# Optimization experiments

Hardware: AMD Instinct MI355X
Metric: run time of the kernel (lower is better)

Reference implementation:

```python
import jax, jax.numpy as jnp
import numpy as np

NG, ND, CIN = 100000, 50000, 128
H, D = 8, 32
HID = H * D
E = 200000
SCALE = 1.0 / np.sqrt(D)


def _segment_softmax(logits, seg, num):
    # logits: [E, H]; softmax over edges sharing the same destination node
    m = jax.ops.segment_max(logits, seg, num_segments=num)
    m = jnp.where(jnp.isfinite(m), m, 0.0)  # guard empty segments
    e = jnp.exp(logits - m[seg])
    s = jax.ops.segment_sum(e, seg, num_segments=num)
    return e / (s[seg] + 1e-16)


def _kqv(x, Wk, bk, Wq, bq, Wv, bv):
    n = x.shape[0]
    return ((x @ Wk + bk).reshape(n, H, D),
            (x @ Wq + bq).reshape(n, H, D),
            (x @ Wv + bv).reshape(n, H, D))


def _message(k_src, v_src, q_dst, src, dst, a_rel, m_rel, p_rel, n_dst):
    # per-edge-type relation transform of gathered K/V, softmax over dst, scatter-add
    k_e = jnp.einsum('ehd,hdf->ehf', k_src[src], a_rel)          # [E,H,D]
    v_e = jnp.einsum('ehd,hdf->ehf', v_src[src], m_rel)          # [E,H,D]
    logits = jnp.einsum('ehf,ehf->eh', q_dst[dst], k_e) * p_rel * SCALE
    alpha = _segment_softmax(logits, dst, n_dst)                 # [E,H]
    return jax.ops.segment_sum(alpha[..., None] * v_e, dst, num_segments=n_dst)


def _forward(x_gene, x_disease, Win_g, bin_g, Wk_g, bk_g, Wq_g, bq_g, Wv_g, bv_g,
             Wa_g, ba_g, skip_g, Win_d, bin_d, Wk_d, bk_d, Wq_d, bq_d, Wv_d, bv_d,
             Wa_d, ba_d, skip_d, a_g2d, m_g2d, p_g2d, a_d2g, m_d2g, p_d2g,
             a_g2g, m_g2g, p_g2g, prelu_w,
             g2d_src, g2d_dst, d2g_src, d2g_dst, g2g_src, g2g_dst):
    # per-type input projection (Encoder.lin_dict)
    xg = x_gene @ Win_g + bin_g      # [NG, HID]
    xd = x_disease @ Win_d + bin_d   # [ND, HID]
    ng, nd = xg.shape[0], xd.shape[0]
    kg, qg, vg = _kqv(xg, Wk_g, bk_g, Wq_g, bq_g, Wv_g, bv_g)
    kd, qd, vd = _kqv(xd, Wk_d, bk_d, Wq_d, bq_d, Wv_d, bv_d)
    # HGTConv: message passing per edge type, summed per destination type
    out_d = _message(kg, vg, qd, g2d_src, g2d_dst, a_g2d, m_g2d, p_g2d, nd)
    out_g = (_message(kd, vd, qg, d2g_src, d2g_dst, a_d2g, m_d2g, p_d2g, ng)
             + _message(kg, vg, qg, g2g_src, g2g_dst, a_g2g, m_g2g, p_g2g, ng))

    def finish(out, x_proj, Wa, ba, skip):
        h = jax.nn.gelu(out.reshape(-1, HID), approximate=False) @ Wa + ba
        beta = jax.nn.sigmoid(skip)
        h = beta * h + (1.0 - beta) * x_proj          # HGT skip connection
        return jnp.where(h > 0, h, prelu_w * h)       # PReLU; Dropout=identity (eval)

    return (finish(out_g, xg, Wa_g, ba_g, skip_g),
            finish(out_d, xd, Wa_d, ba_d, skip_d))


def setup_inputs():
    key = jax.random.key(0)
    ki = iter(jax.random.split(key, 64))
    def nrm(shape, s):
        return (jax.random.normal(next(ki), shape) * s).astype(jnp.float32)
    inp = {}
    inp['x_gene'] = jax.random.normal(next(ki), (NG, CIN), jnp.float32)
    inp['x_disease'] = jax.random.normal(next(ki), (ND, CIN), jnp.float32)
    for t in ('g', 'd'):
        inp[f'Win_{t}'] = nrm((CIN, HID), 0.09)
        inp[f'bin_{t}'] = jnp.zeros((HID,), jnp.float32)
        for p in ('k', 'q', 'v'):
            inp[f'W{p}_{t}'] = nrm((HID, HID), 0.06)
            inp[f'b{p}_{t}'] = jnp.zeros((HID,), jnp.float32)
        inp[f'Wa_{t}'] = nrm((HID, HID), 0.06)
        inp[f'ba_{t}'] = jnp.zeros((HID,), jnp.float32)
        inp[f'skip_{t}'] = jnp.ones((1,), jnp.float32)
    for r in ('g2d', 'd2g', 'g2g'):
        inp[f'a_{r}'] = nrm((H, D, D), 0.18)
        inp[f'm_{r}'] = nrm((H, D, D), 0.18)
        inp[f'p_{r}'] = jnp.ones((H,), jnp.float32)
    inp['prelu_w'] = jnp.full((HID,), 0.25, jnp.float32)
    sizes = {'g2d': (NG, ND), 'd2g': (ND, NG), 'g2g': (NG, NG)}
    for r, (ns_, nd_) in sizes.items():
        inp[f'{r}_src'] = jax.random.randint(next(ki), (E,), 0, ns_, jnp.int32)
        inp[f'{r}_dst'] = jax.random.randint(next(ki), (E,), 0, nd_, jnp.int32)
    return inp


def reference(x_gene, x_disease, Win_g, bin_g, Wk_g, bk_g, Wq_g, bq_g, Wv_g, bv_g,
              Wa_g, ba_g, skip_g, Win_d, bin_d, Wk_d, bk_d, Wq_d, bq_d, Wv_d, bv_d,
              Wa_d, ba_d, skip_d, a_g2d, m_g2d, p_g2d, a_d2g, m_d2g, p_d2g,
              a_g2g, m_g2g, p_g2g, prelu_w,
              g2d_src, g2d_dst, d2g_src, d2g_dst, g2g_src, g2g_dst):
    return _forward(x_gene, x_disease, Win_g, bin_g, Wk_g, bk_g, Wq_g, bq_g, Wv_g, bv_g,
                    Wa_g, ba_g, skip_g, Win_d, bin_d, Wk_d, bk_d, Wq_d, bq_d, Wv_d, bv_d,
                    Wa_d, ba_d, skip_d, a_g2d, m_g2d, p_g2d, a_d2g, m_d2g, p_d2g,
                    a_g2g, m_g2g, p_g2g, prelu_w,
                    g2d_src, g2d_dst, d2g_src, d2g_dst, g2g_src, g2g_dst)
```

## Files before the change

### kernel.cpp

```cpp
#include <hip/hip_runtime.h>
#include <hip/hip_bf16.h>
#include <math.h>

typedef unsigned short u16;
typedef __attribute__((ext_vector_type(4))) float f32x4;
typedef __attribute__((ext_vector_type(8))) short s16x8;

__device__ __forceinline__ float b2f(u16 u){
  union { unsigned u; float f; } v; v.u = ((unsigned)u) << 16; return v.f;
}
__device__ __forceinline__ u16 f2b(float f){
  union { float f; unsigned u; } v; v.f = f;
  unsigned r = v.u + 0x7fffu + ((v.u >> 16) & 1u);
  return (u16)(r >> 16);
}

__device__ __forceinline__ void gload_lds(const u16* g, u16* l){
  __builtin_amdgcn_global_load_lds(
      (const __attribute__((address_space(1))) unsigned*)g,
      (__attribute__((address_space(3))) unsigned*)l, 16, 0, 0);
}

__device__ __forceinline__ int chunk_swz(int bid, int nwg){
  int q = nwg >> 3, r = nwg & 7;
  int xcd = bid & 7, off = bid >> 3;
  return (xcd < r ? xcd*(q+1) : r*(q+1) + (xcd-r)*q) + off;
}

__global__ void zero_k(int* __restrict__ p, int n){
  int i = blockIdx.x*256 + threadIdx.x;
  if(i < n) p[i] = 0;
}

struct T6 { const float* W[6]; u16* O[6]; int K[6]; };
__global__ void transpose6(T6 a){
  int r = blockIdx.y;
  int idx = blockIdx.x*256 + threadIdx.x;
  int K = a.K[r];
  if(idx < K*256){ int k = idx >> 8, n = idx & 255; a.O[r][n*K + k] = f2b(a.W[r][idx]); }
}

struct F6 { const float* Wk[6]; const float* A[6]; u16* O[6]; };
__global__ void foldw6(F6 fa){
  int r = blockIdx.y;
  int idx = blockIdx.x*256 + threadIdx.x;
  int n = idx >> 8, k = idx & 255;
  int h = n >> 5, f = n & 31;
  const float* Wk = fa.Wk[r]; const float* A = fa.A[r];
  float s = 0.f;
  #pragma unroll 8
  for(int d = 0; d < 32; d++)
    s += Wk[k*256 + h*32 + d] * A[h*1024 + d*32 + f];
  fa.O[r][n*256 + k] = f2b(s);
}

struct Fb6 { const float* bk[6]; const float* A[6]; float* O[6]; };
__global__ void foldb6(Fb6 fa){
  int r = blockIdx.x;
  int n = threadIdx.x;
  int h = n >> 5, f = n & 31;
  float s = 0.f;
  for(int d = 0; d < 32; d++)
    s += fa.bk[r][h*32 + d] * fa.A[r][h*1024 + d*32 + f];
  fa.O[r][n] = s;
}

struct CSR3 {
  const int* src[3]; const int* dst[3]; int n[3];
  int* cnt[3]; int* rs[3]; int* cur[3]; int* col[3]; int* tot[3];
};
__global__ void count3(CSR3 c, int E){
  int r = blockIdx.y;
  int e = blockIdx.x*256 + threadIdx.x;
  if(e < E) atomicAdd(&c.cnt[r][c.dst[r][e]], 1);
}
__global__ void alloc3(CSR3 c){
  int r = blockIdx.y;
  int i = blockIdx.x*256 + threadIdx.x;
  if(i < c.n[r]) c.rs[r][i] = atomicAdd(c.tot[r], c.cnt[r][i]);
}
__global__ void fill3(CSR3 c, int E){
  int r = blockIdx.y;
  int e = blockIdx.x*256 + threadIdx.x;
  if(e < E){
    int d = c.dst[r][e];
    int p = c.rs[r][d] + atomicAdd(&c.cur[r][d], 1);
    c.col[r][p] = c.src[r][e];
  }
}

struct GMD {
  const void* A; const u16* BT; const float* bias; void* C;
  int M, K, lda, ldc, lgy, base, epi;
};
struct GM4 { GMD g[4]; int n, nblk; };

template<int AF>
__global__ __launch_bounds__(256) void gemm_multi(GM4 P){
  __shared__ u16 sh[128*64];
  u16* As = sh;
  u16* Bs = sh + 128*32;
  const int t = threadIdx.x;
  const int l = chunk_swz(blockIdx.x, P.nblk);
  int g = 0;
  #pragma unroll
  for(int i = 1; i < 4; i++) if(i < P.n && l >= P.g[i].base) g = i;
  const GMD d = P.g[g];
  const int local = l - d.base;
  const int x = local >> d.lgy;
  const int y = local & ((1 << d.lgy) - 1);
  const int m0 = x << 7, n0 = y << 7;
  const int M = d.M, K = d.K, lda = d.lda, ldc = d.ldc;
  const int w = t >> 6, lane = t & 63;
  const int wm = (w >> 1) << 6;
  const int wn = (w & 1) << 6;
  const int lr = lane & 15, lq = lane >> 4;
  const int jr = lane >> 2;
  const int sp = lane & 3;
  f32x4 acc[4][4];
  #pragma unroll
  for(int i=0;i<4;i++)
    #pragma unroll
    for(int j=0;j<4;j++) acc[i][j] = (f32x4){0.f,0.f,0.f,0.f};

  for(int k0 = 0; k0 < K; k0 += 32){
    if(AF){
      const float* Af = (const float*)d.A;
      #pragma unroll
      for(int j = 0; j < 2; j++){
        int s = t + j*256;
        int rr = s >> 2, p2 = s & 3;
        int sl = p2 ^ (rr & 3);
        int gm = m0 + rr; if(gm > M-1) gm = M-1;
        const float* gp = Af + (size_t)gm*lda + k0 + sl*8;
        float4 f0 = *(const float4*)gp;
        float4 f1 = *(const float4*)(gp + 4);
        s16x8 v;
        v[0]=(short)f2b(f0.x); v[1]=(short)f2b(f0.y); v[2]=(short)f2b(f0.z); v[3]=(short)f2b(f0.w);
        v[4]=(short)f2b(f1.x); v[5]=(short)f2b(f1.y); v[6]=(short)f2b(f1.z); v[7]=(short)f2b(f1.w);
        *(s16x8*)&As[rr*32 + p2*8] = v;
      }
    } else {
      const u16* Ab = (const u16*)d.A;
      #pragma unroll
      for(int i = 0; i < 2; i++){
        int rr = w*32 + i*16 + jr;
        int sl = sp ^ (rr & 3);
        int gm = m0 + rr; if(gm > M-1) gm = M-1;
        gload_lds(Ab + (size_t)gm*lda + k0 + sl*8, &As[(w*32 + i*16)*32]);
      }
    }
    #pragma unroll
    for(int i = 0; i < 2; i++){
      int rr = w*32 + i*16 + jr;
      int sl = sp ^ (rr & 3);
      gload_lds(d.BT + (size_t)(n0 + rr)*K + k0 + sl*8, &Bs[(w*32 + i*16)*32]);
    }
    __syncthreads();
    s16x8 a[4], b[4];
    #pragma unroll
    for(int mt=0; mt<4; mt++)
      a[mt] = *(const s16x8*)&As[(wm + mt*16 + lr)*32 + ((lq ^ (lr&3)) << 3)];
    #pragma unroll
    for(int nt=0; nt<4; nt++)
      b[nt] = *(const s16x8*)&Bs[(wn + nt*16 + lr)*32 + ((lq ^ (lr&3)) << 3)];
    #pragma unroll
    for(int mt=0; mt<4; mt++)
      #pragma unroll
      for(int nt=0; nt<4; nt++)
        acc[mt][nt] = __builtin_amdgcn_mfma_f32_16x16x32_bf16(a[mt], b[nt], acc[mt][nt], 0, 0, 0);
    __syncthreads();
  }

  if(d.epi == 1){
    float* C = (float*)d.C;
    #pragma unroll
    for(int nt=0; nt<4; nt++){
      const int col = n0 + wn + nt*16 + lr;
      const float bc = d.bias[col];
      #pragma unroll
      for(int mt=0; mt<4; mt++)
        #pragma unroll
        for(int i=0;i<4;i++){
          int row = m0 + wm + mt*16 + lq*4 + i;
          if(row < M) C[(size_t)row*ldc + col] = acc[mt][nt][i] + bc;
        }
    }
  } else {
    u16* C = (u16*)d.C;
    #pragma unroll
    for(int p = 0; p < 2; p++){
      if((w & 1) == p){
        #pragma unroll
        for(int nt=0; nt<4; nt++){
          const int cp = nt*16 + lr;
          const float bc = d.bias[n0 + p*64 + cp];
          #pragma unroll
          for(int mt=0; mt<4; mt++)
            #pragma unroll
            for(int i=0;i<4;i++){
              int row = wm + mt*16 + lq*4 + i;
              int so = (cp >> 3) ^ (row & 7);
              sh[row*64 + so*8 + (cp & 7)] = f2b(acc[mt][nt][i] + bc);
            }
        }
      }
      __syncthreads();
      {
        int row = t >> 1, hh = t & 1;
        if(m0 + row < M){
          u16* dst = C + (size_t)(m0 + row)*ldc + n0 + p*64 + hh*32;
          #pragma unroll
          for(int j=0;j<4;j++){
            int so = (hh*4 + j) ^ (row & 7);
            *(s16x8*)(dst + j*8) = *(const s16x8*)&sh[row*64 + so*8];
          }
        }
      }
      __syncthreads();
    }
  }
}

struct GE { const u16* A; const u16* BT; const float* bias; float* C;
            const u16* X; const float* skip; const float* prelu; int M, base; };
struct GE2 { GE g[2]; int nblk; };

__global__ __launch_bounds__(256) void gemm_epi2(GE2 P){
  __shared__ u16 As[64*32];
  __shared__ u16 Bs[256*32];
  const int t = threadIdx.x;
  const int l = chunk_swz(blockIdx.x, P.nblk);
  const int g = (l >= P.g[1].base) ? 1 : 0;
  const GE d = P.g[g];
  const int m0 = (l - d.base) << 6;
  const int M = d.M;
  const int w = t >> 6, lane = t & 63;
  const int wn = w << 6;
  const int lr = lane & 15, lq = lane >> 4;
  const int jr = lane >> 2, sp = lane & 3;
  f32x4 acc[4][4];
  #pragma unroll
  for(int i=0;i<4;i++)
    #pragma unroll
    for(int j=0;j<4;j++) acc[i][j] = (f32x4){0.f,0.f,0.f,0.f};

  for(int k0 = 0; k0 < 256; k0 += 32){
    {
      int rr = w*16 + jr;
      int sl = sp ^ (rr & 3);
      int gm = m0 + rr; if(gm > M-1) gm = M-1;
      gload_lds(d.A + (size_t)gm*512 + k0 + sl*8, &As[(w*16)*32]);
    }
    #pragma unroll
    for(int i = 0; i < 4; i++){
      int rr = w*64 + i*16 + jr;
      int sl = sp ^ (rr & 3);
      gload_lds(d.BT + (size_t)rr*256 + k0 + sl*8, &Bs[(w*64 + i*16)*32]);
    }
    __syncthreads();
    s16x8 a[4], b[4];
    #pragma unroll
    for(int mt=0; mt<4; mt++)
      a[mt] = *(const s16x8*)&As[(mt*16 + lr)*32 + ((lq ^ (lr&3)) << 3)];
    #pragma unroll
    for(int nt=0; nt<4; nt++)
      b[nt] = *(const s16x8*)&Bs[(wn + nt*16 + lr)*32 + ((lq ^ (lr&3)) << 3)];
    #pragma unroll
    for(int mt=0; mt<4; mt++)
      #pragma unroll
      for(int nt=0; nt<4; nt++)
        acc[mt][nt] = __builtin_amdgcn_mfma_f32_16x16x32_bf16(a[mt], b[nt], acc[mt][nt], 0, 0, 0);
    __syncthreads();
  }

  const float beta = 1.f/(1.f + __expf(-d.skip[0]));
  #pragma unroll
  for(int nt=0; nt<4; nt++){
    const int col = wn + nt*16 + lr;
    const float bc = d.bias[col];
    const float pw = d.prelu[col];
    #pragma unroll
    for(int mt=0; mt<4; mt++){
      #pragma unroll
      for(int i=0;i<4;i++){
        int row = m0 + mt*16 + lq*4 + i;
        if(row < M){
          float v = acc[mt][nt][i] + bc;
          float xv = b2f(d.X[(size_t)row*256 + col]);
          v = beta*v + (1.f - beta)*xv;
          v = v > 0.f ? v : pw*v;
          d.C[(size_t)row*256 + col] = v;
        }
      }
    }
  }
}

template<int NREL>
__global__ __launch_bounds__(256) void message_gelu_k(
    const u16* __restrict__ KV1, const float* __restrict__ p1,
    const int* __restrict__ rs1, const int* __restrict__ cnt1, const int* __restrict__ col1,
    const u16* __restrict__ KV2, const float* __restrict__ p2,
    const int* __restrict__ rs2, const int* __restrict__ cnt2, const int* __restrict__ col2,
    float* __restrict__ Qio, int n_dst)
{
  int node = (blockIdx.x << 2) + (threadIdx.x >> 6);
  if(node >= n_dst) return;
  int lane = threadIdx.x & 63;
  float4 qv = *(const float4*)(Qio + (size_t)node*256 + (lane << 2));
  float q0=qv.x, q1=qv.y, q2=qv.z, q3=qv.w;
  float o0=0.f, o1=0.f, o2=0.f, o3=0.f;
  #pragma unroll
  for(int rel = 0; rel < NREL; rel++){
    const u16* KV = rel ? KV2 : KV1;
    const float* pr = rel ? p2 : p1;
    const int* rs = rel ? rs2 : rs1;
    const int* cn = rel ? cnt2 : cnt1;
    const int* cl = rel ? col2 : col1;
    float ps = pr[lane >> 3] * 0.17677669529663687f;
    float a0=0.f,a1=0.f,a2=0.f,a3=0.f,ss=0.f,mx=-1e30f;
    int r0 = rs[node], deg = cn[node];
    int i = 0;
    for(; i + 2 <= deg; i += 2){
      const u16* e0 = KV + (size_t)cl[r0+i]  *512 + (lane<<2);
      const u16* e1 = KV + (size_t)cl[r0+i+1]*512 + (lane<<2);
      ushort4 ka = *(const ushort4*)e0;
      ushort4 va = *(const ushort4*)(e0 + 256);
      ushort4 kb = *(const ushort4*)e1;
      ushort4 vb = *(const ushort4*)(e1 + 256);
      float da = q0*b2f(ka.x) + q1*b2f(ka.y) + q2*b2f(ka.z) + q3*b2f(ka.w);
      float db = q0*b2f(kb.x) + q1*b2f(kb.y) + q2*b2f(kb.z) + q3*b2f(kb.w);
      da += __shfl_xor(da, 1); da += __shfl_xor(da, 2); da += __shfl_xor(da, 4);
      db += __shfl_xor(db, 1); db += __shfl_xor(db, 2); db += __shfl_xor(db, 4);
      float la = da * ps, lb = db * ps;
      float nm = fmaxf(mx, fmaxf(la, lb));
      float c  = __expf(mx - nm);
      float wa = __expf(la - nm);
      float wb = __expf(lb - nm);
      mx = nm;
      ss = ss*c + wa + wb;
      a0 = a0*c + wa*b2f(va.x) + wb*b2f(vb.x);
      a1 = a1*c + wa*b2f(va.y) + wb*b2f(vb.y);
      a2 = a2*c + wa*b2f(va.z) + wb*b2f(vb.z);
      a3 = a3*c + wa*b2f(va.w) + wb*b2f(vb.w);
    }
    if(i < deg){
      const u16* e0 = KV + (size_t)cl[r0+i]*512 + (lane<<2);
      ushort4 ka = *(const ushort4*)e0;
      ushort4 va = *(const ushort4*)(e0 + 256);
      float da = q0*b2f(ka.x) + q1*b2f(ka.y) + q2*b2f(ka.z) + q3*b2f(ka.w);
      da += __shfl_xor(da, 1); da += __shfl_xor(da, 2); da += __shfl_xor(da, 4);
      float la = da * ps;
      float nm = fmaxf(mx, la);
      float c  = __expf(mx - nm);
      float wa = __expf(la - nm);
      mx = nm;
      ss = ss*c + wa;
      a0 = a0*c + wa*b2f(va.x);
      a1 = a1*c + wa*b2f(va.y);
      a2 = a2*c + wa*b2f(va.z);
      a3 = a3*c + wa*b2f(va.w);
    }
    float inv = 1.f/(ss + 1e-16f);
    o0 += a0*inv; o1 += a1*inv; o2 += a2*inv; o3 += a3*inv;
  }
  const float c = 0.70710678118654752f;
  float g0 = 0.5f*o0*(1.f + erff(o0*c));
  float g1 = 0.5f*o1*(1.f + erff(o1*c));
  float g2 = 0.5f*o2*(1.f + erff(o2*c));
  float g3 = 0.5f*o3*(1.f + erff(o3*c));
  ushort4 ov;
  ov.x = f2b(g0); ov.y = f2b(g1); ov.z = f2b(g2); ov.w = f2b(g3);
  *(ushort4*)((u16*)Qio + (size_t)node*512 + (lane << 2)) = ov;
}

extern "C" void kernel_launch(void* const* d_in, const int* in_sizes, int n_in,
                              void* d_out, int out_size, void* d_ws, size_t ws_size,
                              hipStream_t stream)
{
  (void)n_in; (void)out_size; (void)ws_size;
  #define IN_F32(i) ((const float*)d_in[i])
  #define IN_I32(i) ((const int*)d_in[i])
  const int NG = in_sizes[0] / 128;
  const int ND = in_sizes[1] / 128;
  const int E  = in_sizes[34];

  char* p = (char*)d_ws;
  auto carve = [&](size_t bytes) -> void* {
    void* q = (void*)p; p += (bytes + 255) & ~(size_t)255; return q;
  };
  u16* XG   = (u16*)carve((size_t)NG*256*2);
  u16* XD   = (u16*)carve((size_t)ND*256*2);
  u16* KVG  = (u16*)carve((size_t)NG*512*2);
  u16* KVD  = (u16*)carve((size_t)ND*512*2);
  u16* WTinG = (u16*)carve(256*128*2);
  u16* WTinD = (u16*)carve(256*128*2);
  u16* WTqG  = (u16*)carve(256*256*2);
  u16* WTqD  = (u16*)carve(256*256*2);
  u16* WTaG  = (u16*)carve(256*256*2);
  u16* WTaD  = (u16*)carve(256*256*2);
  u16* KVW[3]; for(int i=0;i<3;i++) KVW[i] = (u16*)carve(512*256*2);
  float* FBV[3]; for(int i=0;i<3;i++) FBV[i] = (float*)carve(512*4);
  const int zn = 2*(ND + 2*NG) + 8;
  int* zone = (int*)carve((size_t)zn*4);
  int* cnt0 = zone;
  int* cnt1 = cnt0 + ND;
  int* cnt2 = cnt1 + NG;
  int* cur0 = cnt2 + NG;
  int* cur1 = cur0 + ND;
  int* cur2 = cur1 + NG;
  int* tot  = cur2 + NG;
  int* rs0 = (int*)carve((size_t)ND*4);
  int* rs1 = (int*)carve((size_t)NG*4);
  int* rs2 = (int*)carve((size_t)NG*4);
  int* col0 = (int*)carve((size_t)E*4);
  int* col1 = (int*)carve((size_t)E*4);
  int* col2 = (int*)carve((size_t)E*4);

  float* QGio = (float*)d_out;
  float* QDio = (float*)d_out + (size_t)NG*256;

  {
    T6 a;
    const int wi[6] = {2,13,6,17,10,21};
    u16* wo[6] = {WTinG, WTinD, WTqG, WTqD, WTaG, WTaD};
    const int kk[6] = {128,128,256,256,256,256};
    for(int i=0;i<6;i++){ a.W[i]=IN_F32(wi[i]); a.O[i]=wo[i]; a.K[i]=kk[i]; }
    transpose6<<<dim3(256,6), 256, 0, stream>>>(a);
  }
  {
    F6 a; Fb6 b;
    const int wk[6] = {4,8,15,19,4,8};
    const int bk[6] = {5,9,16,20,5,9};
    const int am[6] = {24,25,27,28,30,31};
    for(int i=0;i<6;i++){
      a.Wk[i]=IN_F32(wk[i]); a.A[i]=IN_F32(am[i]);
      a.O[i] = KVW[i>>1] + (size_t)(i & 1)*256*256;
      b.bk[i]=IN_F32(bk[i]); b.A[i]=IN_F32(am[i]);
      b.O[i] = FBV[i>>1] + (i & 1)*256;
    }
    foldw6<<<dim3(256,6), 256, 0, stream>>>(a);
    foldb6<<<6, 256, 0, stream>>>(b);
  }
  CSR3 c;
  c.src[0]=IN_I32(34); c.dst[0]=IN_I32(35); c.n[0]=ND;
  c.src[1]=IN_I32(36); c.dst[1]=IN_I32(37); c.n[1]=NG;
  c.src[2]=IN_I32(38); c.dst[2]=IN_I32(39); c.n[2]=NG;
  c.cnt[0]=cnt0; c.cnt[1]=cnt1; c.cnt[2]=cnt2;
  c.cur[0]=cur0; c.cur[1]=cur1; c.cur[2]=cur2;
  c.rs[0]=rs0; c.rs[1]=rs1; c.rs[2]=rs2;
  c.col[0]=col0; c.col[1]=col1; c.col[2]=col2;
  c.tot[0]=tot; c.tot[1]=tot+1; c.tot[2]=tot+2;
  const int eb = (E + 255) / 256;
  const int nb = (NG + 255) / 256;
  zero_k<<<(zn + 255) / 256, 256, 0, stream>>>(zone, zn);
  count3<<<dim3(eb,3), 256, 0, stream>>>(c, E);
  alloc3<<<dim3(nb,3), 256, 0, stream>>>(c);
  fill3<<<dim3(eb,3), 256, 0, stream>>>(c, E);

  const int xg = (NG + 127)/128, xd = (ND + 127)/128;

  {
    GM4 pj{};
    pj.g[0].A = d_in[0]; pj.g[0].BT = WTinG; pj.g[0].bias = IN_F32(3);  pj.g[0].C = XG;
    pj.g[0].M = NG; pj.g[0].K = 128; pj.g[0].lda = 128; pj.g[0].ldc = 256;
    pj.g[0].lgy = 1; pj.g[0].base = 0; pj.g[0].epi = 0;
    pj.g[1].A = d_in[1]; pj.g[1].BT = WTinD; pj.g[1].bias = IN_F32(14); pj.g[1].C = XD;
    pj.g[1].M = ND; pj.g[1].K = 128; pj.g[1].lda = 128; pj.g[1].ldc = 256;
    pj.g[1].lgy = 1; pj.g[1].base = xg*2; pj.g[1].epi = 0;
    pj.n = 2; pj.nblk = xg*2 + xd*2;
    gemm_multi<1><<<pj.nblk, 256, 0, stream>>>(pj);
  }

  {
    GM4 md{};
    md.g[0].A = XD; md.g[0].BT = WTqD;   md.g[0].bias = IN_F32(18); md.g[0].C = QDio;
    md.g[0].M = ND; md.g[0].K = 256; md.g[0].lda = 256; md.g[0].ldc = 256;
    md.g[0].lgy = 1; md.g[0].base = 0; md.g[0].epi = 1;
    int b1 = xd*2;
    md.g[1].A = XG; md.g[1].BT = KVW[0]; md.g[1].bias = FBV[0]; md.g[1].C = KVG;
    md.g[1].M = NG; md.g[1].K = 256; md.g[1].lda = 256; md.g[1].ldc = 512;
    md.g[1].lgy = 2; md.g[1].base = b1; md.g[1].epi = 0;
    int b2 = b1 + xg*4;
    md.g[2].A = XG; md.g[2].BT = WTqG;   md.g[2].bias = IN_F32(7); md.g[2].C = QGio;
    md.g[2].M = NG; md.g[2].K = 256; md.g[2].lda = 256; md.g[2].ldc = 256;
    md.g[2].lgy = 1; md.g[2].base = b2; md.g[2].epi = 1;
    int b3 = b2 + xg*2;
    md.g[3].A = XD; md.g[3].BT = KVW[1]; md.g[3].bias = FBV[1]; md.g[3].C = KVD;
    md.g[3].M = ND; md.g[3].K = 256; md.g[3].lda = 256; md.g[3].ldc = 512;
    md.g[3].lgy = 2; md.g[3].base = b3; md.g[3].epi = 0;
    md.n = 4; md.nblk = b3 + xd*4;
    gemm_multi<0><<<md.nblk, 256, 0, stream>>>(md);
  }

  message_gelu_k<1><<<(ND + 3) / 4, 256, 0, stream>>>(
      KVG, IN_F32(26), rs0, cnt0, col0,
      nullptr, nullptr, nullptr, nullptr, nullptr,
      QDio, ND);

  {
    GM4 k2{};
    k2.g[0].A = XG; k2.g[0].BT = KVW[2]; k2.g[0].bias = FBV[2]; k2.g[0].C = KVG;
    k2.g[0].M = NG; k2.g[0].K = 256; k2.g[0].lda = 256; k2.g[0].ldc = 512;
    k2.g[0].lgy = 2; k2.g[0].base = 0; k2.g[0].epi = 0;
    k2.n = 1; k2.nblk = xg*4;
    gemm_multi<0><<<k2.nblk, 256, 0, stream>>>(k2);
  }

  message_gelu_k<2><<<(NG + 3) / 4, 256, 0, stream>>>(
      KVD, IN_F32(29), rs1, cnt1, col1,
      KVG, IN_F32(32), rs2, cnt2, col2,
      QGio, NG);

  {
    GE2 ep{};
    ep.g[0].A = (const u16*)QGio; ep.g[0].BT = WTaG; ep.g[0].bias = IN_F32(11);
    ep.g[0].C = QGio; ep.g[0].X = XG; ep.g[0].skip = IN_F32(12); ep.g[0].prelu = IN_F32(33);
    ep.g[0].M = NG; ep.g[0].base = 0;
    ep.g[1].A = (const u16*)QDio; ep.g[1].BT = WTaD; ep.g[1].bias = IN_F32(22);
    ep.g[1].C = QDio; ep.g[1].X = XD; ep.g[1].skip = IN_F32(23); ep.g[1].prelu = IN_F32(33);
    ep.g[1].M = ND; ep.g[1].base = (NG + 63)/64;
    ep.nblk = (NG + 63)/64 + (ND + 63)/64;
    gemm_epi2<<<ep.nblk, 256, 0, stream>>>(ep);
  }
  #undef IN_F32
  #undef IN_I32
}
```

Measured before the change: 1.043 ms.

## Double-buffer LDS tiles in bf16 GEMM kernels to overlap loads with MFMA

Adds a two-stage LDS ping-pong to the bf16-input path of gemm_multi and to gemm_epi2. The next K-slice is issued with global_load_lds while MFMAs run on the current slice, using explicit waitcnt, barrier and setprio. This targets global-load latency exposed between iterations, at the cost of doubled shared memory per block, which may reduce occupancy. The fp32-input path is left single-buffered.

```diff
diff --git a/kernel.cpp b/kernel.cpp
--- a/kernel.cpp
+++ b/kernel.cpp
@@ -97,9 +97,7 @@
 
 template<int AF>
 __global__ __launch_bounds__(256) void gemm_multi(GM4 P){
-  __shared__ u16 sh[128*64];
-  u16* As = sh;
-  u16* Bs = sh + 128*32;
+  __shared__ u16 sh[2][128*64];
   const int t = threadIdx.x;
   const int l = chunk_swz(blockIdx.x, P.nblk);
   int g = 0;
@@ -123,8 +121,10 @@
     #pragma unroll
     for(int j=0;j<4;j++) acc[i][j] = (f32x4){0.f,0.f,0.f,0.f};
 
-  for(int k0 = 0; k0 < K; k0 += 32){
-    if(AF){
+  if(AF){
+    u16* As = sh[0];
+    u16* Bs = sh[0] + 128*32;
+    for(int k0 = 0; k0 < K; k0 += 32){
       const float* Af = (const float*)d.A;
       #pragma unroll
       for(int j = 0; j < 2; j++){
@@ -140,36 +140,77 @@
         v[4]=(short)f2b(f1.x); v[5]=(short)f2b(f1.y); v[6]=(short)f2b(f1.z); v[7]=(short)f2b(f1.w);
         *(s16x8*)&As[rr*32 + p2*8] = v;
       }
-    } else {
-      const u16* Ab = (const u16*)d.A;
+      #pragma unroll
+      for(int i = 0; i < 2; i++){
+        int rr = w*32 + i*16 + jr;
+        int sl = sp ^ (rr & 3);
+        gload_lds(d.BT + (size_t)(n0 + rr)*K + k0 + sl*8, &Bs[(w*32 + i*16)*32]);
+      }
+      __syncthreads();
+      s16x8 a[4], b[4];
+      #pragma unroll
+      for(int mt=0; mt<4; mt++)
+        a[mt] = *(const s16x8*)&As[(wm + mt*16 + lr)*32 + ((lq ^ (lr&3)) << 3)];
+      #pragma unroll
+      for(int nt=0; nt<4; nt++)
+        b[nt] = *(const s16x8*)&Bs[(wn + nt*16 + lr)*32 + ((lq ^ (lr&3)) << 3)];
+      #pragma unroll
+      for(int mt=0; mt<4; mt++)
+        #pragma unroll
+        for(int nt=0; nt<4; nt++)
+          acc[mt][nt] = __builtin_amdgcn_mfma_f32_16x16x32_bf16(a[mt], b[nt], acc[mt][nt], 0, 0, 0);
+      __syncthreads();
+    }
+  } else {
+    const u16* Ab = (const u16*)d.A;
+    auto stage = [&](int kk, int bi){
+      u16* As = sh[bi];
+      u16* Bs = sh[bi] + 128*32;
       #pragma unroll
       for(int i = 0; i < 2; i++){
         int rr = w*32 + i*16 + jr;
         int sl = sp ^ (rr & 3);
         int gm = m0 + rr; if(gm > M-1) gm = M-1;
-        gload_lds(Ab + (size_t)gm*lda + k0 + sl*8, &As[(w*32 + i*16)*32]);
-      }
-    }
-    #pragma unroll
-    for(int i = 0; i < 2; i++){
-      int rr = w*32 + i*16 + jr;
-      int sl = sp ^ (rr & 3);
-      gload_lds(d.BT + (size_t)(n0 + rr)*K + k0 + sl*8, &Bs[(w*32 + i*16)*32]);
-    }
-    __syncthreads();
-    s16x8 a[4], b[4];
-    #pragma unroll
-    for(int mt=0; mt<4; mt++)
-      a[mt] = *(const s16x8*)&As[(wm + mt*16 + lr)*32 + ((lq ^ (lr&3)) << 3)];
-    #pragma unroll
-    for(int nt=0; nt<4; nt++)
-      b[nt] = *(const s16x8*)&Bs[(wn + nt*16 + lr)*32 + ((lq ^ (lr&3)) << 3)];
-    #pragma unroll
-    for(int mt=0; mt<4; mt++)
-      #pragma unroll
-      for(int nt=0; nt<4; nt++)
-        acc[mt][nt] = __builtin_amdgcn_mfma_f32_16x16x32_bf16(a[mt], b[nt], acc[mt][nt], 0, 0, 0);
-    __syncthreads();
+        gload_lds(Ab + (size_t)gm*lda + kk + sl*8, &As[(w*32 + i*16)*32]);
+      }
+      #pragma unroll
+      for(int i = 0; i < 2; i++){
+        int rr = w*32 + i*16 + jr;
+        int sl = sp ^ (rr & 3);
+        gload_lds(d.BT + (size_t)(n0 + rr)*K + kk + sl*8, &Bs[(w*32 + i*16)*32]);
+      }
+    };
+    const int nt = K >> 5;
+    int cur = 0;
+    stage(0, 0);
+    asm volatile("s_waitcnt vmcnt(0)" ::: "memory");
+    __builtin_amdgcn_s_barrier();
+    __builtin_amdgcn_sched_barrier(0);
+    for(int ts = 0; ts < nt; ++ts){
+      if(ts + 1 < nt) stage((ts+1) << 5, cur ^ 1);
+      const u16* As = sh[cur];
+      const u16* Bs = sh[cur] + 128*32;
+      s16x8 a[4], b[4];
+      #pragma unroll
+      for(int mt=0; mt<4; mt++)
+        a[mt] = *(const s16x8*)&As[(wm + mt*16 + lr)*32 + ((lq ^ (lr&3)) << 3)];
+      #pragma unroll
+      for(int nn=0; nn<4; nn++)
+        b[nn] = *(const s16x8*)&Bs[(wn + nn*16 + lr)*32 + ((lq ^ (lr&3)) << 3)];
+      asm volatile("s_waitcnt lgkmcnt(0)" ::: "memory");
+      __builtin_amdgcn_sched_barrier(0);
+      __builtin_amdgcn_s_setprio(1);
+      #pragma unroll
+      for(int mt=0; mt<4; mt++)
+        #pragma unroll
+        for(int nn=0; nn<4; nn++)
+          acc[mt][nn] = __builtin_amdgcn_mfma_f32_16x16x32_bf16(a[mt], b[nn], acc[mt][nn], 0, 0, 0);
+      __builtin_amdgcn_s_setprio(0);
+      asm volatile("s_waitcnt vmcnt(0)" ::: "memory");
+      __builtin_amdgcn_s_barrier();
+      __builtin_amdgcn_sched_barrier(0);
+      cur ^= 1;
+    }
   }
 
   if(d.epi == 1){
@@ -187,6 +228,7 @@
         }
     }
   } else {
+    u16* shm = sh[0];
     u16* C = (u16*)d.C;
     #pragma unroll
     for(int p = 0; p < 2; p++){
@@ -201,7 +243,7 @@
             for(int i=0;i<4;i++){
               int row = wm + mt*16 + lq*4 + i;
               int so = (cp >> 3) ^ (row & 7);
-              sh[row*64 + so*8 + (cp & 7)] = f2b(acc[mt][nt][i] + bc);
+              shm[row*64 + so*8 + (cp & 7)] = f2b(acc[mt][nt][i] + bc);
             }
         }
       }
@@ -213,7 +255,7 @@
           #pragma unroll
           for(int j=0;j<4;j++){
             int so = (hh*4 + j) ^ (row & 7);
-            *(s16x8*)(dst + j*8) = *(const s16x8*)&sh[row*64 + so*8];
+            *(s16x8*)(dst + j*8) = *(const s16x8*)&shm[row*64 + so*8];
           }
         }
       }
@@ -227,8 +269,8 @@
 struct GE2 { GE g[2]; int nblk; };
 
 __global__ __launch_bounds__(256) void gemm_epi2(GE2 P){
-  __shared__ u16 As[64*32];
-  __shared__ u16 Bs[256*32];
+  __shared__ u16 Abuf[2][64*32];
+  __shared__ u16 Bbuf[2][256*32];
   const int t = threadIdx.x;
   const int l = chunk_swz(blockIdx.x, P.nblk);
   const int g = (l >= P.g[1].base) ? 1 : 0;
@@ -245,33 +287,49 @@
     #pragma unroll
     for(int j=0;j<4;j++) acc[i][j] = (f32x4){0.f,0.f,0.f,0.f};
 
-  for(int k0 = 0; k0 < 256; k0 += 32){
+  auto stage = [&](int kk, int bi){
     {
       int rr = w*16 + jr;
       int sl = sp ^ (rr & 3);
       int gm = m0 + rr; if(gm > M-1) gm = M-1;
-      gload_lds(d.A + (size_t)gm*512 + k0 + sl*8, &As[(w*16)*32]);
+      gload_lds(d.A + (size_t)gm*512 + kk + sl*8, &Abuf[bi][(w*16)*32]);
     }
     #pragma unroll
     for(int i = 0; i < 4; i++){
       int rr = w*64 + i*16 + jr;
       int sl = sp ^ (rr & 3);
-      gload_lds(d.BT + (size_t)rr*256 + k0 + sl*8, &Bs[(w*64 + i*16)*32]);
-    }
-    __syncthreads();
+      gload_lds(d.BT + (size_t)rr*256 + kk + sl*8, &Bbuf[bi][(w*64 + i*16)*32]);
+    }
+  };
+  int cur = 0;
+  stage(0, 0);
+  asm volatile("s_waitcnt vmcnt(0)" ::: "memory");
+  __builtin_amdgcn_s_barrier();
+  __builtin_amdgcn_sched_barrier(0);
+  for(int ts = 0; ts < 8; ++ts){
+    if(ts + 1 < 8) stage((ts+1) << 5, cur ^ 1);
+    const u16* As = Abuf[cur];
+    const u16* Bs = Bbuf[cur];
     s16x8 a[4], b[4];
     #pragma unroll
     for(int mt=0; mt<4; mt++)
       a[mt] = *(const s16x8*)&As[(mt*16 + lr)*32 + ((lq ^ (lr&3)) << 3)];
     #pragma unroll
-    for(int nt=0; nt<4; nt++)
-      b[nt] = *(const s16x8*)&Bs[(wn + nt*16 + lr)*32 + ((lq ^ (lr&3)) << 3)];
+    for(int nn=0; nn<4; nn++)
+      b[nn] = *(const s16x8*)&Bs[(wn + nn*16 + lr)*32 + ((lq ^ (lr&3)) << 3)];
+    asm volatile("s_waitcnt lgkmcnt(0)" ::: "memory");
+    __builtin_amdgcn_sched_barrier(0);
+    __builtin_amdgcn_s_setprio(1);
     #pragma unroll
     for(int mt=0; mt<4; mt++)
       #pragma unroll
-      for(int nt=0; nt<4; nt++)
-        acc[mt][nt] = __builtin_amdgcn_mfma_f32_16x16x32_bf16(a[mt], b[nt], acc[mt][nt], 0, 0, 0);
-    __syncthreads();
+      for(int nn=0; nn<4; nn++)
+        acc[mt][nn] = __builtin_amdgcn_mfma_f32_16x16x32_bf16(a[mt], b[nn], acc[mt][nn], 0, 0, 0);
+    __builtin_amdgcn_s_setprio(0);
+    asm volatile("s_waitcnt vmcnt(0)" ::: "memory");
+    __builtin_amdgcn_s_barrier();
+    __builtin_amdgcn_sched_barrier(0);
+    cur ^= 1;
   }
 
   const float beta = 1.f/(1.f + __expf(-d.skip[0]));
```

New measurement: 1.018 ms. 1.02x faster.

## Keep A row-tile resident in LDS and sweep all weight panels per block

Applied to the files above, without the earlier changes.

Replaces the multi-GEMM K/Q/V projection launch with a kernel in which each block loads its full 128x256 row strip of the activations into LDS once, then loops over all output column panels, reading B fragments directly from global memory. When workspace allows, the g2g K/V projection goes into a separate buffer and is folded into the same launch, removing a later launch and a second read of XG. The output GEMM likewise keeps its whole A strip in LDS and drops the per-K-step barriers. In exchange it uses much more LDS per block, which lowers occupancy, and it relies on B being served well from cache without staging.

```diff
diff --git a/kernel.cpp b/kernel.cpp
--- a/kernel.cpp
+++ b/kernel.cpp
@@ -93,18 +93,16 @@
   const void* A; const u16* BT; const float* bias; void* C;
   int M, K, lda, ldc, lgy, base, epi;
 };
-struct GM4 { GMD g[4]; int n, nblk; };
+struct GM5 { GMD g[5]; int n, nblk; };
 
 template<int AF>
-__global__ __launch_bounds__(256) void gemm_multi(GM4 P){
-  __shared__ u16 sh[128*64];
-  u16* As = sh;
-  u16* Bs = sh + 128*32;
+__global__ __launch_bounds__(256) void gemm_multi(GM5 P){
+  __shared__ u16 sh[2][128*64];
   const int t = threadIdx.x;
   const int l = chunk_swz(blockIdx.x, P.nblk);
   int g = 0;
   #pragma unroll
-  for(int i = 1; i < 4; i++) if(i < P.n && l >= P.g[i].base) g = i;
+  for(int i = 1; i < 5; i++) if(i < P.n && l >= P.g[i].base) g = i;
   const GMD d = P.g[g];
   const int local = l - d.base;
   const int x = local >> d.lgy;
@@ -115,16 +113,17 @@
   const int wm = (w >> 1) << 6;
   const int wn = (w & 1) << 6;
   const int lr = lane & 15, lq = lane >> 4;
-  const int jr = lane >> 2;
-  const int sp = lane & 3;
   f32x4 acc[4][4];
   #pragma unroll
   for(int i=0;i<4;i++)
     #pragma unroll
     for(int j=0;j<4;j++) acc[i][j] = (f32x4){0.f,0.f,0.f,0.f};
 
-  for(int k0 = 0; k0 < K; k0 += 32){
-    if(AF){
+  {
+    u16* As = sh[0];
+    u16* Bs = sh[0] + 128*32;
+    const int jr = lane >> 2, sp = lane & 3;
+    for(int k0 = 0; k0 < K; k0 += 32){
       const float* Af = (const float*)d.A;
       #pragma unroll
       for(int j = 0; j < 2; j++){
@@ -140,84 +139,173 @@
         v[4]=(short)f2b(f1.x); v[5]=(short)f2b(f1.y); v[6]=(short)f2b(f1.z); v[7]=(short)f2b(f1.w);
         *(s16x8*)&As[rr*32 + p2*8] = v;
       }
-    } else {
-      const u16* Ab = (const u16*)d.A;
       #pragma unroll
       for(int i = 0; i < 2; i++){
         int rr = w*32 + i*16 + jr;
         int sl = sp ^ (rr & 3);
-        int gm = m0 + rr; if(gm > M-1) gm = M-1;
-        gload_lds(Ab + (size_t)gm*lda + k0 + sl*8, &As[(w*32 + i*16)*32]);
-      }
-    }
-    #pragma unroll
-    for(int i = 0; i < 2; i++){
-      int rr = w*32 + i*16 + jr;
-      int sl = sp ^ (rr & 3);
-      gload_lds(d.BT + (size_t)(n0 + rr)*K + k0 + sl*8, &Bs[(w*32 + i*16)*32]);
-    }
-    __syncthreads();
-    s16x8 a[4], b[4];
-    #pragma unroll
-    for(int mt=0; mt<4; mt++)
-      a[mt] = *(const s16x8*)&As[(wm + mt*16 + lr)*32 + ((lq ^ (lr&3)) << 3)];
-    #pragma unroll
-    for(int nt=0; nt<4; nt++)
-      b[nt] = *(const s16x8*)&Bs[(wn + nt*16 + lr)*32 + ((lq ^ (lr&3)) << 3)];
-    #pragma unroll
-    for(int mt=0; mt<4; mt++)
+        gload_lds(d.BT + (size_t)(n0 + rr)*K + k0 + sl*8, &Bs[(w*32 + i*16)*32]);
+      }
+      __syncthreads();
+      s16x8 a[4], b[4];
+      #pragma unroll
+      for(int mt=0; mt<4; mt++)
+        a[mt] = *(const s16x8*)&As[(wm + mt*16 + lr)*32 + ((lq ^ (lr&3)) << 3)];
       #pragma unroll
       for(int nt=0; nt<4; nt++)
-        acc[mt][nt] = __builtin_amdgcn_mfma_f32_16x16x32_bf16(a[mt], b[nt], acc[mt][nt], 0, 0, 0);
-    __syncthreads();
-  }
-
-  if(d.epi == 1){
-    float* C = (float*)d.C;
-    #pragma unroll
-    for(int nt=0; nt<4; nt++){
-      const int col = n0 + wn + nt*16 + lr;
-      const float bc = d.bias[col];
+        b[nt] = *(const s16x8*)&Bs[(wn + nt*16 + lr)*32 + ((lq ^ (lr&3)) << 3)];
       #pragma unroll
       for(int mt=0; mt<4; mt++)
         #pragma unroll
-        for(int i=0;i<4;i++){
-          int row = m0 + wm + mt*16 + lq*4 + i;
-          if(row < M) C[(size_t)row*ldc + col] = acc[mt][nt][i] + bc;
+        for(int nt=0; nt<4; nt++)
+          acc[mt][nt] = __builtin_amdgcn_mfma_f32_16x16x32_bf16(a[mt], b[nt], acc[mt][nt], 0, 0, 0);
+      __syncthreads();
+    }
+  }
+
+  u16* shm = sh[0];
+  u16* C = (u16*)d.C;
+  #pragma unroll
+  for(int p = 0; p < 2; p++){
+    if((w & 1) == p){
+      #pragma unroll
+      for(int nt=0; nt<4; nt++){
+        const int cp = nt*16 + lr;
+        const float bc = d.bias[n0 + p*64 + cp];
+        #pragma unroll
+        for(int mt=0; mt<4; mt++)
+          #pragma unroll
+          for(int i=0;i<4;i++){
+            int row = wm + mt*16 + lq*4 + i;
+            int so = (cp >> 3) ^ (row & 7);
+            shm[row*64 + so*8 + (cp & 7)] = f2b(acc[mt][nt][i] + bc);
+          }
+      }
+    }
+    __syncthreads();
+    {
+      int row = t >> 1, hh = t & 1;
+      if(m0 + row < M){
+        u16* dst = C + (size_t)(m0 + row)*ldc + n0 + p*64 + hh*32;
+        #pragma unroll
+        for(int j=0;j<4;j++){
+          int so = (hh*4 + j) ^ (row & 7);
+          *(s16x8*)(dst + j*8) = *(const s16x8*)&shm[row*64 + so*8];
         }
-    }
-  } else {
-    u16* C = (u16*)d.C;
+      }
+    }
+    __syncthreads();
+  }
+}
+
+struct Panel { const u16* BT; const float* bias; void* C; int ldc, epi; };
+struct Mega { const u16* A[2]; int M[2]; int np[2]; int pb[2]; int split; Panel p[16]; };
+
+__global__ __launch_bounds__(256) void gemm_mega(Mega P){
+  __shared__ u16 As[128*256];
+  __shared__ u16 Cs[128*64];
+  const int t = threadIdx.x;
+  const int blk = blockIdx.x;
+  const int side = (blk >= P.split) ? 1 : 0;
+  const u16* A = P.A[side];
+  const int M = P.M[side];
+  const int np = P.np[side];
+  const int pb = P.pb[side];
+  const int m0 = (side ? blk - P.split : blk) << 7;
+  const int w = t >> 6, lane = t & 63;
+  const int wm = (w >> 1) << 6;
+  const int wn = (w & 1) << 6;
+  const int lr = lane & 15, lq = lane >> 4;
+
+  #pragma unroll
+  for(int i = 0; i < 16; i++){
+    int rbase = w*32 + i*2;
+    int rr = rbase + (lane >> 5);
+    int sp = lane & 31;
+    int sl = sp ^ (rr & 7);
+    int gm = m0 + rr; if(gm > M-1) gm = M-1;
+    gload_lds(A + (size_t)gm*256 + sl*8, &As[rbase*256]);
+  }
+  asm volatile("s_waitcnt vmcnt(0)" ::: "memory");
+  __syncthreads();
+
+  for(int p = 0; p < np; p++){
+    const u16* Bp = P.p[pb + p].BT;
+    const float* bias = P.p[pb + p].bias;
+    void* Cp = P.p[pb + p].C;
+    const int ldc = P.p[pb + p].ldc;
+    const int epi = P.p[pb + p].epi;
+    f32x4 acc[4][4];
     #pragma unroll
-    for(int p = 0; p < 2; p++){
-      if((w & 1) == p){
+    for(int i=0;i<4;i++)
+      #pragma unroll
+      for(int j=0;j<4;j++) acc[i][j] = (f32x4){0.f,0.f,0.f,0.f};
+
+    #pragma unroll 2
+    for(int ts = 0; ts < 8; ts++){
+      s16x8 b[4], a[4];
+      #pragma unroll
+      for(int nt=0;nt<4;nt++)
+        b[nt] = *(const s16x8*)&Bp[(size_t)(wn + nt*16 + lr)*256 + ts*32 + lq*8];
+      #pragma unroll
+      for(int mt=0;mt<4;mt++){
+        int ra = wm + mt*16 + lr;
+        int ps = (ts*4 + lq) ^ (ra & 7);
+        a[mt] = *(const s16x8*)&As[ra*256 + ps*8];
+      }
+      #pragma unroll
+      for(int mt=0;mt<4;mt++)
         #pragma unroll
-        for(int nt=0; nt<4; nt++){
-          const int cp = nt*16 + lr;
-          const float bc = d.bias[n0 + p*64 + cp];
+        for(int nt=0;nt<4;nt++)
+          acc[mt][nt] = __builtin_amdgcn_mfma_f32_16x16x32_bf16(a[mt], b[nt], acc[mt][nt], 0, 0, 0);
+    }
+
+    if(epi == 1){
+      float* C = (float*)Cp;
+      #pragma unroll
+      for(int nt=0; nt<4; nt++){
+        const int col = wn + nt*16 + lr;
+        const float bc = bias[col];
+        #pragma unroll
+        for(int mt=0; mt<4; mt++)
           #pragma unroll
-          for(int mt=0; mt<4; mt++)
+          for(int i=0;i<4;i++){
+            int row = m0 + wm + mt*16 + lq*4 + i;
+            if(row < M) C[(size_t)row*ldc + col] = acc[mt][nt][i] + bc;
+          }
+      }
+    } else {
+      u16* C = (u16*)Cp;
+      #pragma unroll
+      for(int p2 = 0; p2 < 2; p2++){
+        if((w & 1) == p2){
+          #pragma unroll
+          for(int nt=0; nt<4; nt++){
+            const int cp = nt*16 + lr;
+            const float bc = bias[p2*64 + cp];
             #pragma unroll
-            for(int i=0;i<4;i++){
-              int row = wm + mt*16 + lq*4 + i;
-              int so = (cp >> 3) ^ (row & 7);
-              sh[row*64 + so*8 + (cp & 7)] = f2b(acc[mt][nt][i] + bc);
-            }
-        }
-      }
-      __syncthreads();
-      {
-        int row = t >> 1, hh = t & 1;
-        if(m0 + row < M){
-          u16* dst = C + (size_t)(m0 + row)*ldc + n0 + p*64 + hh*32;
-          #pragma unroll
-          for(int j=0;j<4;j++){
-            int so = (hh*4 + j) ^ (row & 7);
-            *(s16x8*)(dst + j*8) = *(const s16x8*)&sh[row*64 + so*8];
+            for(int mt=0; mt<4; mt++)
+              #pragma unroll
+              for(int i=0;i<4;i++){
+                int row = wm + mt*16 + lq*4 + i;
+                int so = (cp >> 3) ^ (row & 7);
+                Cs[row*64 + so*8 + (cp & 7)] = f2b(acc[mt][nt][i] + bc);
+              }
           }
         }
-      }
-      __syncthreads();
+        __syncthreads();
+        {
+          int row = t >> 1, hh = t & 1;
+          if(m0 + row < M){
+            u16* dst = C + (size_t)(m0 + row)*ldc + p2*64 + hh*32;
+            #pragma unroll
+            for(int j=0;j<4;j++){
+              int so = (hh*4 + j) ^ (row & 7);
+              *(s16x8*)(dst + j*8) = *(const s16x8*)&Cs[row*64 + so*8];
+            }
+          }
+        }
+        __syncthreads();
+      }
     }
   }
 }
@@ -227,8 +315,7 @@
 struct GE2 { GE g[2]; int nblk; };
 
 __global__ __launch_bounds__(256) void gemm_epi2(GE2 P){
-  __shared__ u16 As[64*32];
-  __shared__ u16 Bs[256*32];
+  __shared__ u16 As[64*256];
   const int t = threadIdx.x;
   const int l = chunk_swz(blockIdx.x, P.nblk);
   const int g = (l >= P.g[1].base) ? 1 : 0;
@@ -238,40 +325,42 @@
   const int w = t >> 6, lane = t & 63;
   const int wn = w << 6;
   const int lr = lane & 15, lq = lane >> 4;
-  const int jr = lane >> 2, sp = lane & 3;
+
+  #pragma unroll
+  for(int i = 0; i < 8; i++){
+    int rbase = w*16 + i*2;
+    int rr = rbase + (lane >> 5);
+    int sp = lane & 31;
+    int sl = sp ^ (rr & 7);
+    int gm = m0 + rr; if(gm > M-1) gm = M-1;
+    gload_lds(d.A + (size_t)gm*512 + sl*8, &As[rbase*256]);
+  }
+  asm volatile("s_waitcnt vmcnt(0)" ::: "memory");
+  __syncthreads();
+
   f32x4 acc[4][4];
   #pragma unroll
   for(int i=0;i<4;i++)
     #pragma unroll
     for(int j=0;j<4;j++) acc[i][j] = (f32x4){0.f,0.f,0.f,0.f};
 
-  for(int k0 = 0; k0 < 256; k0 += 32){
-    {
-      int rr = w*16 + jr;
-      int sl = sp ^ (rr & 3);
-      int gm = m0 + rr; if(gm > M-1) gm = M-1;
-      gload_lds(d.A + (size_t)gm*512 + k0 + sl*8, &As[(w*16)*32]);
-    }
-    #pragma unroll
-    for(int i = 0; i < 4; i++){
-      int rr = w*64 + i*16 + jr;
-      int sl = sp ^ (rr & 3);
-      gload_lds(d.BT + (size_t)rr*256 + k0 + sl*8, &Bs[(w*64 + i*16)*32]);
-    }
-    __syncthreads();
+  #pragma unroll 2
+  for(int ts = 0; ts < 8; ts++){
     s16x8 a[4], b[4];
     #pragma unroll
-    for(int mt=0; mt<4; mt++)
-      a[mt] = *(const s16x8*)&As[(mt*16 + lr)*32 + ((lq ^ (lr&3)) << 3)];
+    for(int nt=0;nt<4;nt++)
+      b[nt] = *(const s16x8*)&d.BT[(size_t)(wn + nt*16 + lr)*256 + ts*32 + lq*8];
     #pragma unroll
-    for(int nt=0; nt<4; nt++)
-      b[nt] = *(const s16x8*)&Bs[(wn + nt*16 + lr)*32 + ((lq ^ (lr&3)) << 3)];
+    for(int mt=0;mt<4;mt++){
+      int ra = mt*16 + lr;
+      int ps = (ts*4 + lq) ^ (ra & 7);
+      a[mt] = *(const s16x8*)&As[ra*256 + ps*8];
+    }
     #pragma unroll
-    for(int mt=0; mt<4; mt++)
-      #pragma unroll
-      for(int nt=0; nt<4; nt++)
+    for(int mt=0;mt<4;mt++)
+      #pragma unroll
+      for(int nt=0;nt<4;nt++)
         acc[mt][nt] = __builtin_amdgcn_mfma_f32_16x16x32_bf16(a[mt], b[nt], acc[mt][nt], 0, 0, 0);
-    __syncthreads();
   }
 
   const float beta = 1.f/(1.f + __expf(-d.skip[0]));
@@ -379,7 +468,7 @@
                               void* d_out, int out_size, void* d_ws, size_t ws_size,
                               hipStream_t stream)
 {
-  (void)n_in; (void)out_size; (void)ws_size;
+  (void)n_in; (void)out_size;
   #define IN_F32(i) ((const float*)d_in[i])
   #define IN_I32(i) ((const int*)d_in[i])
   const int NG = in_sizes[0] / 128;
@@ -417,6 +506,12 @@
   int* col0 = (int*)carve((size_t)E*4);
   int* col1 = (int*)carve((size_t)E*4);
   int* col2 = (int*)carve((size_t)E*4);
+  u16* KVG2 = nullptr;
+  {
+    size_t used = (size_t)(p - (char*)d_ws);
+    size_t need = (size_t)NG*512*2 + 4096;
+    if(ws_size >= used + need) KVG2 = (u16*)carve((size_t)NG*512*2);
+  }
 
   float* QGio = (float*)d_out;
   float* QDio = (float*)d_out + (size_t)NG*256;
@@ -462,7 +557,7 @@
   const int xg = (NG + 127)/128, xd = (ND + 127)/128;
 
   {
-    GM4 pj{};
+    GM5 pj{};
     pj.g[0].A = d_in[0]; pj.g[0].BT = WTinG; pj.g[0].bias = IN_F32(3);  pj.g[0].C = XG;
     pj.g[0].M = NG; pj.g[0].K = 128; pj.g[0].lda = 128; pj.g[0].ldc = 256;
     pj.g[0].lgy = 1; pj.g[0].base = 0; pj.g[0].epi = 0;
@@ -473,25 +568,34 @@
     gemm_multi<1><<<pj.nblk, 256, 0, stream>>>(pj);
   }
 
+  auto setPanel = [&](Panel& pn, const u16* BT, const float* bias, void* C,
+                      int n0, int ldc, int epi, int elemSize){
+    pn.BT = BT + (size_t)n0*256;
+    pn.bias = bias + n0;
+    pn.C = (char*)C + (size_t)n0*elemSize;
+    pn.ldc = ldc; pn.epi = epi;
+  };
   {
-    GM4 md{};
-    md.g[0].A = XD; md.g[0].BT = WTqD;   md.g[0].bias = IN_F32(18); md.g[0].C = QDio;
-    md.g[0].M = ND; md.g[0].K = 256; md.g[0].lda = 256; md.g[0].ldc = 256;
-    md.g[0].lgy = 1; md.g[0].base = 0; md.g[0].epi = 1;
-    int b1 = xd*2;
-    md.g[1].A = XG; md.g[1].BT = KVW[0]; md.g[1].bias = FBV[0]; md.g[1].C = KVG;
-    md.g[1].M = NG; md.g[1].K = 256; md.g[1].lda = 256; md.g[1].ldc = 512;
-    md.g[1].lgy = 2; md.g[1].base = b1; md.g[1].epi = 0;
-    int b2 = b1 + xg*4;
-    md.g[2].A = XG; md.g[2].BT = WTqG;   md.g[2].bias = IN_F32(7); md.g[2].C = QGio;
-    md.g[2].M = NG; md.g[2].K = 256; md.g[2].lda = 256; md.g[2].ldc = 256;
-    md.g[2].lgy = 1; md.g[2].base = b2; md.g[2].epi = 1;
-    int b3 = b2 + xg*2;
-    md.g[3].A = XD; md.g[3].BT = KVW[1]; md.g[3].bias = FBV[1]; md.g[3].C = KVD;
-    md.g[3].M = ND; md.g[3].K = 256; md.g[3].lda = 256; md.g[3].ldc = 512;
-    md.g[3].lgy = 2; md.g[3].base = b3; md.g[3].epi = 0;
-    md.n = 4; md.nblk = b3 + xd*4;
-    gemm_multi<0><<<md.nblk, 256, 0, stream>>>(md);
+    Mega mg{};
+    mg.A[0] = XG; mg.M[0] = NG; mg.pb[0] = 0;
+    mg.A[1] = XD; mg.M[1] = ND; mg.pb[1] = 10;
+    mg.split = xg;
+    int gp = 0;
+    for(int n0 = 0; n0 < 512; n0 += 128)
+      setPanel(mg.p[gp++], KVW[0], FBV[0], KVG, n0, 512, 0, 2);
+    for(int n0 = 0; n0 < 256; n0 += 128)
+      setPanel(mg.p[gp++], WTqG, IN_F32(7), QGio, n0, 256, 1, 4);
+    if(KVG2)
+      for(int n0 = 0; n0 < 512; n0 += 128)
+        setPanel(mg.p[gp++], KVW[2], FBV[2], KVG2, n0, 512, 0, 2);
+    mg.np[0] = gp;
+    int dp = 10;
+    for(int n0 = 0; n0 < 256; n0 += 128)
+      setPanel(mg.p[dp++], WTqD, IN_F32(18), QDio, n0, 256, 1, 4);
+    for(int n0 = 0; n0 < 512; n0 += 128)
+      setPanel(mg.p[dp++], KVW[1], FBV[1], KVD, n0, 512, 0, 2);
+    mg.np[1] = dp - 10;
+    gemm_mega<<<xg + xd, 256, 0, stream>>>(mg);
   }
 
   message_gelu_k<1><<<(ND + 3) / 4, 256, 0, stream>>>(
@@ -499,18 +603,21 @@
       nullptr, nullptr, nullptr, nullptr, nullptr,
       QDio, ND);
 
-  {
-    GM4 k2{};
-    k2.g[0].A = XG; k2.g[0].BT = KVW[2]; k2.g[0].bias = FBV[2]; k2.g[0].C = KVG;
-    k2.g[0].M = NG; k2.g[0].K = 256; k2.g[0].lda = 256; k2.g[0].ldc = 512;
-    k2.g[0].lgy = 2; k2.g[0].base = 0; k2.g[0].epi = 0;
-    k2.n = 1; k2.nblk = xg*4;
-    gemm_multi<0><<<k2.nblk, 256, 0, stream>>>(k2);
+  if(!KVG2){
+    Mega mg{};
+    mg.A[0] = XG; mg.M[0] = NG; mg.pb[0] = 0;
+    mg.A[1] = XG; mg.M[1] = NG; mg.pb[1] = 10;
+    mg.split = xg;
+    int gp = 0;
+    for(int n0 = 0; n0 < 512; n0 += 128)
+      setPanel(mg.p[gp++], KVW[2], FBV[2], KVG, n0, 512, 0, 2);
+    mg.np[0] = gp; mg.np[1] = 0;
+    gemm_mega<<<xg, 256, 0, stream>>>(mg);
   }
 
   message_gelu_k<2><<<(NG + 3) / 4, 256, 0, stream>>>(
       KVD, IN_F32(29), rs1, cnt1, col1,
-      KVG, IN_F32(32), rs2, cnt2, col2,
+      KVG2 ? KVG2 : KVG, IN_F32(32), rs2, cnt2, col2,
       QGio, NG);
 
   {
```

Result: slower. 1.145 ms (+9.8%).
